# Kernel optimization log

Hardware: AMD Instinct MI355X
Metric: run time of the kernel (lower is better)

The kernel has to match this reference:

```python
import jax, jax.numpy as jnp
import numpy as np

# Problem sizes
P = 4096            # number of distinct property ids (segment domain)
N = 16_777_216      # number of value tokens in batch

# PropertyLossTracker hyperparameters (from __init__ defaults)
POWER = 0.5
EMA_DECAY = 0.99
MIN_FREQ = 1e-5
WARMUP_BATCHES = 1000
SLOW_WARMUP = 3000
MAX_WEIGHT = 30.0
RAMP_BATCHES = 200


def setup_inputs() -> dict:
    key = jax.random.key(0)
    k1, k2, k3 = jax.random.split(key, 3)
    property_ids = jax.random.randint(k1, (N,), 0, P)
    # CE-like nonnegative per-token losses
    token_losses = jax.random.uniform(k2, (N,), dtype=jnp.float32) * 5.0
    # EMA frequency state (dense vector replacing the defaultdict)
    prop_freq = jax.random.uniform(k3, (P,), dtype=jnp.float32) * 0.01 + MIN_FREQ
    return {
        "property_ids": property_ids,
        "token_losses": token_losses,
        "prop_freq": prop_freq,
        "batch_counter": 5000,  # > slow_warmup: steady-state weighting branch
    }


def reference(property_ids, token_losses, prop_freq, batch_counter):
    # --- fused segment reductions (replaces python loop over unique ids) ---
    ones = jnp.ones_like(token_losses)
    counts = jax.ops.segment_sum(ones, property_ids, num_segments=P)          # [P]
    sums = jax.ops.segment_sum(token_losses, property_ids, num_segments=P)    # [P]
    present = counts > 0
    # per-property mean loss (masked segment-mean)
    mean_loss = jnp.where(present, sums / jnp.maximum(counts, 1.0), 0.0)

    # --- EMA frequency update (decay all, add batch freq for present props) ---
    n_tokens = jnp.asarray(token_losses.shape[0], dtype=jnp.float32)
    batch_freq = counts / (n_tokens + 1e-6)
    new_freq = prop_freq * EMA_DECAY + jnp.where(present, (1.0 - EMA_DECAY) * batch_freq, 0.0)

    # --- inverse-frequency weights ---
    freq_cl = jnp.maximum(new_freq, MIN_FREQ)
    raw = 1.0 / (freq_cl + 1e-6) ** POWER
    ramp = jnp.minimum(1.0, (batch_counter - WARMUP_BATCHES) / RAMP_BATCHES)
    raw = 1.0 + ramp * (raw - 1.0)
    raw = jnp.minimum(MAX_WEIGHT, raw)
    # slow-warmup blend branch
    frac = batch_counter / SLOW_WARMUP
    raw = jnp.where(batch_counter <= SLOW_WARMUP, raw * frac + (1.0 - frac), raw)
    raw = jnp.where(batch_counter <= WARMUP_BATCHES, 1.0, raw)

    w = jnp.where(present, raw, 0.0)
    w = w / (w.sum() + 1e-6)

    stratified_loss = (mean_loss * w).sum()
    unweighted_loss = token_losses.mean()
    return stratified_loss, unweighted_loss, new_freq
```

## Files before the change

kernel.cpp:

```cpp
#include <hip/hip_runtime.h>

#define NPROP 4096
#define NTOK  16777216
#define BLOCK 1024
#define GRID  512
#define NREP  8
#define STRIDE (GRID * BLOCK)
#define ROUNDS (NTOK / 4 / STRIDE)

#define CSHIFT32 23
#define FXP_SCALE 2048.0f
#define INV_FXP   (1.0f / 2048.0f)

#define CSHIFT64 39
#define SUM_MASK64 ((1ULL << CSHIFT64) - 1)


__global__ __launch_bounds__(BLOCK) void hist_kernel(
    const int* __restrict__ ids, const float* __restrict__ losses,
    unsigned long long* __restrict__ g_rep)
{
    __shared__ unsigned s_hist[NPROP];
    for (int i = threadIdx.x; i < NPROP; i += BLOCK) s_hist[i] = 0u;
    __syncthreads();

    const int4*   ids4 = (const int4*)ids;
    const float4* ls4  = (const float4*)losses;
    const int tid = blockIdx.x * BLOCK + threadIdx.x;

#pragma unroll 2
    for (int b = 0; b < ROUNDS; ++b) {
        int i = tid + b * STRIDE;
        int4   id = ids4[i];
        float4 l  = ls4[i];
        atomicAdd(&s_hist[id.x], (1u << CSHIFT32) | (unsigned)(l.x * FXP_SCALE + 0.5f));
        atomicAdd(&s_hist[id.y], (1u << CSHIFT32) | (unsigned)(l.y * FXP_SCALE + 0.5f));
        atomicAdd(&s_hist[id.z], (1u << CSHIFT32) | (unsigned)(l.z * FXP_SCALE + 0.5f));
        atomicAdd(&s_hist[id.w], (1u << CSHIFT32) | (unsigned)(l.w * FXP_SCALE + 0.5f));
    }

    __syncthreads();
    unsigned long long* rep = g_rep + (unsigned)(blockIdx.x & (NREP - 1)) * NPROP;
    for (int i = threadIdx.x; i < NPROP; i += BLOCK) {
        unsigned v = s_hist[i];
        if (v) {
            unsigned long long cnt = (unsigned long long)(v >> CSHIFT32);
            unsigned long long fxp = (unsigned long long)(v & ((1u << CSHIFT32) - 1u));
            atomicAdd(&rep[i], (cnt << CSHIFT64) | fxp);
        }
    }
}

__global__ __launch_bounds__(1024) void finalize_kernel(
    const unsigned long long* __restrict__ g_rep,
    const float* __restrict__ prop_freq, const int* __restrict__ d_bc,
    float* __restrict__ out)
{
    __shared__ float s_raw[16], s_dot[16], s_tot[16];

    const int bc_i = d_bc[0];
    const float bc = (float)bc_i;
    const float ramp = fminf(1.0f, (bc - 1000.0f) / 200.0f);
    const float frac = bc / 3000.0f;

    float a_raw = 0.0f, a_dot = 0.0f, a_tot = 0.0f;

    for (int p = threadIdx.x; p < NPROP; p += 1024) {
        unsigned long long v = 0;
#pragma unroll
        for (int r = 0; r < NREP; ++r)
            v += g_rep[r * NPROP + p];

        float cnt  = (float)(unsigned)(v >> CSHIFT64);
        float sumf = (float)(v & SUM_MASK64) * INV_FXP;
        bool present = cnt > 0.0f;
        a_tot += sumf;

        float mean_loss = present ? sumf / fmaxf(cnt, 1.0f) : 0.0f;
        float batch_freq = cnt / ((float)NTOK + 1e-6f);
        float new_freq = prop_freq[p] * 0.99f + (present ? 0.01f * batch_freq : 0.0f);
        out[2 + p] = new_freq;

        float freq_cl = fmaxf(new_freq, 1e-5f);
        float raw = 1.0f / sqrtf(freq_cl + 1e-6f);
        raw = 1.0f + ramp * (raw - 1.0f);
        raw = fminf(30.0f, raw);
        if (bc_i <= 3000) raw = raw * frac + (1.0f - frac);
        if (bc_i <= 1000) raw = 1.0f;

        float w = present ? raw : 0.0f;
        a_raw += w;
        a_dot += mean_loss * w;
    }

    for (int off = 32; off > 0; off >>= 1) {
        a_raw += __shfl_down(a_raw, off, 64);
        a_dot += __shfl_down(a_dot, off, 64);
        a_tot += __shfl_down(a_tot, off, 64);
    }
    int wave = threadIdx.x >> 6;
    if ((threadIdx.x & 63) == 0) {
        s_raw[wave] = a_raw;
        s_dot[wave] = a_dot;
        s_tot[wave] = a_tot;
    }
    __syncthreads();
    if (threadIdx.x == 0) {
        float t_raw = 0.0f, t_dot = 0.0f, t_tot = 0.0f;
        for (int i = 0; i < 16; ++i) {
            t_raw += s_raw[i];
            t_dot += s_dot[i];
            t_tot += s_tot[i];
        }
        out[0] = t_dot / (t_raw + 1e-6f);
        out[1] = t_tot / (float)NTOK;
    }
}

extern "C" void kernel_launch(void* const* d_in, const int* in_sizes, int n_in,
                              void* d_out, int out_size, void* d_ws, size_t ws_size,
                              hipStream_t stream) {
    const int*   ids       = (const int*)d_in[0];
    const float* losses    = (const float*)d_in[1];
    const float* prop_freq = (const float*)d_in[2];
    const int*   d_bc      = (const int*)d_in[3];
    float* out = (float*)d_out;

    unsigned long long* g_rep = (unsigned long long*)d_ws;

    hipMemsetAsync(d_ws, 0, (size_t)NREP * NPROP * 8, stream);

    hist_kernel<<<GRID, BLOCK, 0, stream>>>(ids, losses, g_rep);
    finalize_kernel<<<1, 1024, 0, stream>>>(g_rep, prop_freq, d_bc, out);
}
```

Measured before the change: 161.7 us.

## Replace shared atomics with per-wave tagged software histograms and prefetch

Each wave now gets its own private LDS histogram. Hardware LDS atomics are replaced by a tag-based read-modify-write retry loop, where each lane stamps its lane id and re-reads to detect collisions. The block size drops to 256, the next round's ids and losses are prefetched, and the loss fixed-point scale is cut to 1/32 so the count and sum fit beside the tag. This aims to remove LDS atomic cost and cross-wave contention. In exchange it uses much more LDS per block, which lowers occupancy, needs three LDS accesses plus a loop per element, and quantizes the losses more coarsely.

```diff
diff --git a/kernel.cpp b/kernel.cpp
--- a/kernel.cpp
+++ b/kernel.cpp
@@ -2,15 +2,20 @@
 
 #define NPROP 4096
 #define NTOK  16777216
-#define BLOCK 1024
+#define BLOCK 256
+#define NWAVES (BLOCK / 64)
 #define GRID  512
 #define NREP  8
 #define STRIDE (GRID * BLOCK)
 #define ROUNDS (NTOK / 4 / STRIDE)
 
-#define CSHIFT32 23
-#define FXP_SCALE 2048.0f
-#define INV_FXP   (1.0f / 2048.0f)
+#define TAG_SHIFT 26
+#define DATA_MASK 0x03FFFFFFu
+#define CSHIFT32 17
+#define CNT_MASK32 0x1FFu
+#define SUM_MASK32 0x1FFFFu
+#define FXP_SCALE 32.0f
+#define INV_FXP   (1.0f / 32.0f)
 
 #define CSHIFT64 39
 #define SUM_MASK64 ((1ULL << CSHIFT64) - 1)
@@ -20,34 +25,56 @@
     const int* __restrict__ ids, const float* __restrict__ losses,
     unsigned long long* __restrict__ g_rep)
 {
-    __shared__ unsigned s_hist[NPROP];
-    for (int i = threadIdx.x; i < NPROP; i += BLOCK) s_hist[i] = 0u;
+    __shared__ unsigned s_hist[NWAVES * NPROP];
+    for (int i = threadIdx.x; i < NWAVES * NPROP; i += BLOCK) s_hist[i] = 0u;
     __syncthreads();
+
+    const int lane = threadIdx.x & 63;
+    const int wave = threadIdx.x >> 6;
+    volatile unsigned* h = s_hist + wave * NPROP;
+    const unsigned mytag = (unsigned)lane << TAG_SHIFT;
 
     const int4*   ids4 = (const int4*)ids;
     const float4* ls4  = (const float4*)losses;
     const int tid = blockIdx.x * BLOCK + threadIdx.x;
 
-#pragma unroll 2
+    int4   id = ids4[tid];
+    float4 l  = ls4[tid];
+
     for (int b = 0; b < ROUNDS; ++b) {
-        int i = tid + b * STRIDE;
-        int4   id = ids4[i];
-        float4 l  = ls4[i];
-        atomicAdd(&s_hist[id.x], (1u << CSHIFT32) | (unsigned)(l.x * FXP_SCALE + 0.5f));
-        atomicAdd(&s_hist[id.y], (1u << CSHIFT32) | (unsigned)(l.y * FXP_SCALE + 0.5f));
-        atomicAdd(&s_hist[id.z], (1u << CSHIFT32) | (unsigned)(l.z * FXP_SCALE + 0.5f));
-        atomicAdd(&s_hist[id.w], (1u << CSHIFT32) | (unsigned)(l.w * FXP_SCALE + 0.5f));
+        int nb = (b + 1) & (ROUNDS - 1);
+        int4   idn = ids4[tid + nb * STRIDE];
+        float4 ln  = ls4[tid + nb * STRIDE];
+
+#pragma unroll
+        for (int u = 0; u < 4; ++u) {
+            int   bin = (u == 0) ? id.x : (u == 1) ? id.y : (u == 2) ? id.z : id.w;
+            float lv  = (u == 0) ? l.x  : (u == 1) ? l.y  : (u == 2) ? l.z  : l.w;
+            unsigned contrib = (1u << CSHIFT32) | (unsigned)(lv * FXP_SCALE + 0.5f);
+            bool pend = true;
+            while (__any(pend)) {
+                if (pend) {
+                    unsigned cur = h[bin];
+                    h[bin] = ((cur & DATA_MASK) + contrib) | mytag;
+                    unsigned chk = h[bin];
+                    if ((chk >> TAG_SHIFT) == (unsigned)lane) pend = false;
+                }
+            }
+        }
+        id = idn; l = ln;
     }
+    __syncthreads();
 
-    __syncthreads();
     unsigned long long* rep = g_rep + (unsigned)(blockIdx.x & (NREP - 1)) * NPROP;
     for (int i = threadIdx.x; i < NPROP; i += BLOCK) {
-        unsigned v = s_hist[i];
-        if (v) {
-            unsigned long long cnt = (unsigned long long)(v >> CSHIFT32);
-            unsigned long long fxp = (unsigned long long)(v & ((1u << CSHIFT32) - 1u));
-            atomicAdd(&rep[i], (cnt << CSHIFT64) | fxp);
+        unsigned c = 0, s = 0;
+#pragma unroll
+        for (int w = 0; w < NWAVES; ++w) {
+            unsigned v = s_hist[w * NPROP + i];
+            c += (v >> CSHIFT32) & CNT_MASK32;
+            s += v & SUM_MASK32;
         }
+        if (c) atomicAdd(&rep[i], ((unsigned long long)c << CSHIFT64) | (unsigned long long)s);
     }
 }
 
@@ -98,11 +125,11 @@
         a_dot += __shfl_down(a_dot, off, 64);
         a_tot += __shfl_down(a_tot, off, 64);
     }
-    int wave = threadIdx.x >> 6;
+    int wv = threadIdx.x >> 6;
     if ((threadIdx.x & 63) == 0) {
-        s_raw[wave] = a_raw;
-        s_dot[wave] = a_dot;
-        s_tot[wave] = a_tot;
+        s_raw[wv] = a_raw;
+        s_dot[wv] = a_dot;
+        s_tot[wv] = a_tot;
     }
     __syncthreads();
     if (threadIdx.x == 0) {
```

Result: slower. 189.4 us (+17.1%).
